# Performance work log

Hardware: AMD Instinct MI355X
Metric: run time of the kernel (lower is better)

Reference implementation:

```python
import jax, jax.numpy as jnp
import numpy as np

N, E = 100000, 1600000
IN_C, HID_C, OUT_C = 128, 64, 40


def setup_inputs() -> dict:
    key = jax.random.key(0)
    ks = jax.random.split(key, 8)
    s = lambda fan_in: 1.0 / np.sqrt(fan_in)
    return {
        "x": jax.random.normal(ks[0], (N, IN_C), dtype=jnp.float32),
        "edge_index": jax.random.randint(ks[1], (2, E), 0, N, dtype=jnp.int64),
        # SAGEConv layer 1: lin_l (on aggregated neighbors, with bias) + lin_r (root, no bias)
        "W_l1": jax.random.uniform(ks[2], (IN_C, HID_C), jnp.float32, -s(IN_C), s(IN_C)),
        "b_l1": jnp.zeros((HID_C,), jnp.float32),
        "W_r1": jax.random.uniform(ks[3], (IN_C, HID_C), jnp.float32, -s(IN_C), s(IN_C)),
        # SAGEConv layer 2
        "W_l2": jax.random.uniform(ks[4], (HID_C, OUT_C), jnp.float32, -s(HID_C), s(HID_C)),
        "b_l2": jnp.zeros((OUT_C,), jnp.float32),
        "W_r2": jax.random.uniform(ks[5], (HID_C, OUT_C), jnp.float32, -s(HID_C), s(HID_C)),
    }


def _sage_conv(x, src, dst, W_l, b_l, W_r, n_nodes):
    # mean-aggregate neighbor features: scatter-add x[src] onto dst, divide by degree
    agg = jax.ops.segment_sum(x[src], dst, num_segments=n_nodes)  # [N, F]
    deg = jax.ops.segment_sum(jnp.ones((src.shape[0],), x.dtype), dst, num_segments=n_nodes)
    mean = agg / jnp.maximum(deg, 1.0)[:, None]
    return mean @ W_l + b_l + x @ W_r


def reference(x, edge_index, W_l1, b_l1, W_r1, W_l2, b_l2, W_r2):
    src, dst = edge_index[0], edge_index[1]  # messages flow src -> dst
    # eval mode: dropout is identity
    hid = _sage_conv(x, src, dst, W_l1, b_l1, W_r1, N)
    hid = jax.nn.relu(hid)
    out = _sage_conv(hid, src, dst, W_l2, b_l2, W_r2, N)
    return jax.nn.log_softmax(out, axis=1)
```

## Files before the change

kernel.cpp:

```cpp
#include <hip/hip_runtime.h>
#include <hip/hip_bf16.h>

#define N_NODES 100000
#define E_EDGES 1600000
#define IN_C 128
#define HID_C 64
#define OUT_C 40

#define NBUCK 196
#define BCAP 9216
#define B1_EPT 16
#define B1_CHUNK (256 * B1_EPT)
#define B1_GRID ((E_EDGES + B1_CHUNK - 1) / B1_CHUNK)
#define TILE_GRID ((N_NODES + 63) / 64)

typedef unsigned short ushort_t;
typedef unsigned int uint_t;
typedef unsigned char uchar_t;
typedef __attribute__((ext_vector_type(8))) short bf16x8;
typedef __attribute__((ext_vector_type(4))) float f32x4;
typedef __attribute__((ext_vector_type(2))) float f32x2;

__device__ __forceinline__ float bfu2f(ushort_t u) {
    return __uint_as_float(((uint_t)u) << 16);
}
__device__ __forceinline__ ushort_t f2bfu(float f) {
    uint_t u = __float_as_uint(f);
    return (ushort_t)((u + 0x7FFFu + ((u >> 16) & 1u)) >> 16);
}
__device__ __forceinline__ uchar_t f2fp8(float f) {
    int p = __builtin_amdgcn_cvt_pk_fp8_f32(f, f, 0, false);
    return (uchar_t)(p & 0xff);
}

struct SmemPrep {
    int cnt[NBUCK];
    int base[NBUCK];
};
struct SmemGemm1 {
    ushort_t xs[64 * 136];
    ushort_t wsm[128 * 136];
};
union SmemK1 {
    SmemPrep p;
    SmemGemm1 g;
};

__global__ __launch_bounds__(256) void k_prep_gemm1(const int* __restrict__ src, const int* __restrict__ dst,
                                                    int* __restrict__ bcur, int* __restrict__ bucket,
                                                    const float* __restrict__ Wl1, const float* __restrict__ Wr1,
                                                    const float* __restrict__ x,
                                                    uchar_t* __restrict__ h1l, ushort_t* __restrict__ h1r) {
    __shared__ SmemK1 sm;
    const int t = threadIdx.x;

    if (blockIdx.x < B1_GRID) {
        const int e0 = blockIdx.x * B1_CHUNK;
        for (int i = t; i < NBUCK; i += 256) sm.p.cnt[i] = 0;
        __syncthreads();

        int myp[B1_EPT];
        int myb[B1_EPT];
#pragma unroll
        for (int j = 0; j < B1_EPT; ++j) {
            int e = e0 + t + j * 256;
            if (e < E_EDGES) {
                int d = dst[e];
                myp[j] = src[e] | ((d & 511) << 17);
                myb[j] = d >> 9;
                atomicAdd(&sm.p.cnt[myb[j]], 1);
            } else {
                myb[j] = -1;
            }
        }
        __syncthreads();
        for (int i = t; i < NBUCK; i += 256) {
            sm.p.base[i] = atomicAdd(&bcur[i], sm.p.cnt[i]);
            sm.p.cnt[i] = 0;
        }
        __syncthreads();
#pragma unroll
        for (int j = 0; j < B1_EPT; ++j) {
            if (myb[j] >= 0) {
                int b = myb[j];
                int loc = atomicAdd(&sm.p.cnt[b], 1);
                int pos = sm.p.base[b] + loc;
                if (pos < BCAP) bucket[(size_t)b * BCAP + pos] = myp[j];
            }
        }
    } else {
        const int row_base = (blockIdx.x - B1_GRID) * 64;

        for (int i = t; i < 128 * 64; i += 256) {
            int n = i & 127, kp = i >> 7;
            const float* W = (n < 64) ? Wl1 : Wr1;
            int nn = n & 63;
            float va = W[(2 * kp) * 64 + nn];
            float vb = W[(2 * kp + 1) * 64 + nn];
            uint_t u = (uint_t)f2bfu(va) | ((uint_t)f2bfu(vb) << 16);
            *(uint_t*)(sm.g.wsm + n * 136 + 2 * kp) = u;
        }
        for (int i = t; i < 64 * 32; i += 256) {
            int row = i >> 5, seg = i & 31;
            int gr = row_base + row;
            float4 v = make_float4(0.f, 0.f, 0.f, 0.f);
            if (gr < N_NODES) v = *(const float4*)(x + (size_t)gr * IN_C + seg * 4);
            ushort4 u;
            u.x = f2bfu(v.x); u.y = f2bfu(v.y); u.z = f2bfu(v.z); u.w = f2bfu(v.w);
            *(ushort4*)(sm.g.xs + row * 136 + seg * 4) = u;
        }
        __syncthreads();

        const int wv = t >> 6, lane = t & 63;
        const int m = lane & 15, quad = lane >> 4;
        const int m0 = wv * 16;

        bf16x8 a[4];
#pragma unroll
        for (int kk = 0; kk < 4; ++kk)
            a[kk] = *(const bf16x8*)(sm.g.xs + (m0 + m) * 136 + kk * 32 + quad * 8);

        f32x4 acc[8];
#pragma unroll
        for (int nt = 0; nt < 8; ++nt) acc[nt] = (f32x4){0.f, 0.f, 0.f, 0.f};

#pragma unroll
        for (int nt = 0; nt < 8; ++nt) {
#pragma unroll
            for (int kk = 0; kk < 4; ++kk) {
                bf16x8 b = *(const bf16x8*)(sm.g.wsm + (nt * 16 + m) * 136 + kk * 32 + quad * 8);
                acc[nt] = __builtin_amdgcn_mfma_f32_16x16x32_bf16(a[kk], b, acc[nt], 0, 0, 0);
            }
        }

        const int grow_base = row_base + m0 + quad * 4;
#pragma unroll
        for (int r = 0; r < 4; ++r) {
            int grow = grow_base + r;
            if (grow < N_NODES) {
#pragma unroll
                for (int nt = 0; nt < 4; ++nt)
                    h1l[(size_t)grow * HID_C + nt * 16 + m] = f2fp8(acc[nt][r]);
#pragma unroll
                for (int nt = 4; nt < 8; ++nt)
                    h1r[(size_t)grow * HID_C + (nt - 4) * 16 + m] = f2bfu(acc[nt][r]);
            }
        }
    }
}

__global__ __launch_bounds__(512) void k_csr(const int* __restrict__ bucket, const int* __restrict__ bcur,
                                             int* __restrict__ rowptr, int* __restrict__ csr,
                                             const float* __restrict__ Wl2, const float* __restrict__ Wr2,
                                             ushort_t* __restrict__ Wt2) {
    const int t = threadIdx.x;
    if (blockIdx.x >= NBUCK) {
        int i = (blockIdx.x - NBUCK) * 512 + t;
        if (i < 80 * 64) {
            int n = i >> 6, k = i & 63;
            float v = (n < 40) ? Wl2[k * 40 + n] : Wr2[k * 40 + (n - 40)];
            Wt2[n * 64 + k] = f2bfu(v);
        }
        return;
    }

    __shared__ int red[512];
    __shared__ int hist[512];
    __shared__ int scan[512];
    __shared__ int cur[512];
    __shared__ int csrbuf[BCAP];

    const int b = blockIdx.x;
    const int n0 = b << 9;
    const int nb = min(512, N_NODES - n0);
    const int sz = min(bcur[b], BCAP);
    const int* bdata = bucket + (size_t)b * BCAP;

    red[t] = (t < b) ? min(bcur[t], BCAP) : 0;
    __syncthreads();
    for (int off = 256; off > 0; off >>= 1) {
        if (t < off) red[t] += red[t + off];
        __syncthreads();
    }
    const int cbase = red[0];

    hist[t] = 0;
    __syncthreads();
    for (int i = t; i < sz; i += 512) atomicAdd(&hist[bdata[i] >> 17], 1);
    __syncthreads();

    scan[t] = hist[t];
    __syncthreads();
    for (int off = 1; off < 512; off <<= 1) {
        int add = (t >= off) ? scan[t - off] : 0;
        __syncthreads();
        scan[t] += add;
        __syncthreads();
    }

    int exc = scan[t] - hist[t];
    cur[t] = exc;
    if (t < nb) rowptr[n0 + t] = cbase + exc;
    __syncthreads();

    for (int i = t; i < sz; i += 512) {
        int p = bdata[i];
        int pos = atomicAdd(&cur[p >> 17], 1);
        csrbuf[pos] = (p & 0x1FFFF) << 6;
    }
    __syncthreads();
    for (int i = t; i < sz; i += 512)
        csr[cbase + i] = csrbuf[i];
    if (b == NBUCK - 1 && t == 0) rowptr[N_NODES] = cbase + sz;
}

__global__ __launch_bounds__(256) void k_agg1_gemm2(const int* __restrict__ rowptr, const int* __restrict__ csr,
                                                    const uchar_t* __restrict__ h1l, const ushort_t* __restrict__ h1r,
                                                    const float* __restrict__ b1, const ushort_t* __restrict__ Wt,
                                                    uchar_t* __restrict__ h2l, ushort_t* __restrict__ h2r) {
    __shared__ ushort_t hs[64 * 72];
    __shared__ ushort_t wsm[80 * 72];
    const int t = threadIdx.x;
    const int row_base = blockIdx.x * 64;
    const int wv = t >> 6, lane = t & 63;
    const int slot = lane >> 3;
    const int part = lane & 7;

    for (int i = t; i < 80 * 8; i += 256) {
        int n = i >> 3, seg = i & 7;
        uint4 v = *(const uint4*)(Wt + n * 64 + seg * 8);
        *(uint4*)(wsm + n * 72 + seg * 8) = v;
    }

    float4 bb0, bb1;
    if (slot == 0) {
        bb0 = *(const float4*)(b1 + part * 8);
        bb1 = *(const float4*)(b1 + part * 8 + 4);
    }
    for (int r16 = 0; r16 < 16; ++r16) {
        int lrow = wv * 16 + r16;
        int row = row_base + lrow;
        if (row < N_NODES) {
            int2 rp = *(const int2*)(rowptr + row);
            int start = rp.x, end = rp.y;
            f32x2 acc[4];
#pragma unroll
            for (int j = 0; j < 4; ++j) acc[j] = (f32x2){0.f, 0.f};

            int base = start;
            for (; base + 8 <= end; base += 8) {
                int s = csr[base + slot];
                uint2 u = *(const uint2*)(h1l + s + part * 8);
                acc[0] += __builtin_amdgcn_cvt_pk_f32_fp8(u.x, false);
                acc[1] += __builtin_amdgcn_cvt_pk_f32_fp8(u.x, true);
                acc[2] += __builtin_amdgcn_cvt_pk_f32_fp8(u.y, false);
                acc[3] += __builtin_amdgcn_cvt_pk_f32_fp8(u.y, true);
            }
            if (base < end) {
                int e = base + slot;
                int s = csr[min(e, end - 1)];
                uint2 u = *(const uint2*)(h1l + s + part * 8);
                if (e >= end) { u.x = 0u; u.y = 0u; }
                acc[0] += __builtin_amdgcn_cvt_pk_f32_fp8(u.x, false);
                acc[1] += __builtin_amdgcn_cvt_pk_f32_fp8(u.x, true);
                acc[2] += __builtin_amdgcn_cvt_pk_f32_fp8(u.y, false);
                acc[3] += __builtin_amdgcn_cvt_pk_f32_fp8(u.y, true);
            }
#pragma unroll
            for (int off = 8; off <= 32; off <<= 1) {
#pragma unroll
                for (int j = 0; j < 4; ++j) {
                    f32x2 tt;
                    tt.x = __shfl_xor(acc[j].x, off);
                    tt.y = __shfl_xor(acc[j].y, off);
                    acc[j] += tt;
                }
            }
            if (slot == 0) {
                float inv = __builtin_amdgcn_rcpf(fmaxf((float)(end - start), 1.0f));
                ushort_t rr[8];
                *(uint4*)rr = *(const uint4*)(h1r + (size_t)row * HID_C + part * 8);
                ushort_t o[8];
                o[0] = f2bfu(fmaxf(acc[0].x * inv + bfu2f(rr[0]) + bb0.x, 0.f));
                o[1] = f2bfu(fmaxf(acc[0].y * inv + bfu2f(rr[1]) + bb0.y, 0.f));
                o[2] = f2bfu(fmaxf(acc[1].x * inv + bfu2f(rr[2]) + bb0.z, 0.f));
                o[3] = f2bfu(fmaxf(acc[1].y * inv + bfu2f(rr[3]) + bb0.w, 0.f));
                o[4] = f2bfu(fmaxf(acc[2].x * inv + bfu2f(rr[4]) + bb1.x, 0.f));
                o[5] = f2bfu(fmaxf(acc[2].y * inv + bfu2f(rr[5]) + bb1.y, 0.f));
                o[6] = f2bfu(fmaxf(acc[3].x * inv + bfu2f(rr[6]) + bb1.z, 0.f));
                o[7] = f2bfu(fmaxf(acc[3].y * inv + bfu2f(rr[7]) + bb1.w, 0.f));
                *(uint4*)(hs + lrow * 72 + part * 8) = *(const uint4*)o;
            }
        } else if (slot == 0) {
            uint4 z = make_uint4(0u, 0u, 0u, 0u);
            *(uint4*)(hs + lrow * 72 + part * 8) = z;
        }
    }
    __syncthreads();

    const int m = lane & 15, quad = lane >> 4;
    const int m0 = wv * 16;

    bf16x8 a[2];
#pragma unroll
    for (int kk = 0; kk < 2; ++kk)
        a[kk] = *(const bf16x8*)(hs + (m0 + m) * 72 + kk * 32 + quad * 8);

    f32x4 acc[5];
#pragma unroll
    for (int nt = 0; nt < 5; ++nt) acc[nt] = (f32x4){0.f, 0.f, 0.f, 0.f};

#pragma unroll
    for (int nt = 0; nt < 5; ++nt) {
#pragma unroll
        for (int kk = 0; kk < 2; ++kk) {
            bf16x8 b = *(const bf16x8*)(wsm + (nt * 16 + m) * 72 + kk * 32 + quad * 8);
            acc[nt] = __builtin_amdgcn_mfma_f32_16x16x32_bf16(a[kk], b, acc[nt], 0, 0, 0);
        }
    }

    const int grow_base = row_base + m0 + quad * 4;
#pragma unroll
    for (int r = 0; r < 4; ++r) {
        int grow = grow_base + r;
        if (grow < N_NODES) {
#pragma unroll
            for (int nt = 0; nt < 5; ++nt) {
                int col = nt * 16 + m;
                float v = acc[nt][r];
                if (col < OUT_C) h2l[(size_t)grow * 64 + col] = f2fp8(v);
                else             h2r[(size_t)grow * OUT_C + (col - OUT_C)] = f2bfu(v);
            }
        }
    }
}

__global__ __launch_bounds__(256) void k_agg2(const int* __restrict__ rowptr, const int* __restrict__ csr,
                                              const uchar_t* __restrict__ h2l, const ushort_t* __restrict__ h2r,
                                              const float* __restrict__ b2, float* __restrict__ out) {
    int row = (blockIdx.x * 256 + threadIdx.x) >> 6;
    int lane = threadIdx.x & 63;
    if (row >= N_NODES) return;
    int2 rp = *(const int2*)(rowptr + row);
    int start = rp.x, end = rp.y;
    const int slot = lane >> 3;
    const int part = lane & 7;
    f32x2 acc[4];
#pragma unroll
    for (int j = 0; j < 4; ++j) acc[j] = (f32x2){0.f, 0.f};

    int base = start;
    for (; base + 8 <= end; base += 8) {
        int s = csr[base + slot];
        uint2 u = *(const uint2*)(h2l + s + part * 8);
        acc[0] += __builtin_amdgcn_cvt_pk_f32_fp8(u.x, false);
        acc[1] += __builtin_amdgcn_cvt_pk_f32_fp8(u.x, true);
        acc[2] += __builtin_amdgcn_cvt_pk_f32_fp8(u.y, false);
        acc[3] += __builtin_amdgcn_cvt_pk_f32_fp8(u.y, true);
    }
    if (base < end) {
        int e = base + slot;
        int s = csr[min(e, end - 1)];
        uint2 u = *(const uint2*)(h2l + s + part * 8);
        if (e >= end) { u.x = 0u; u.y = 0u; }
        acc[0] += __builtin_amdgcn_cvt_pk_f32_fp8(u.x, false);
        acc[1] += __builtin_amdgcn_cvt_pk_f32_fp8(u.x, true);
        acc[2] += __builtin_amdgcn_cvt_pk_f32_fp8(u.y, false);
        acc[3] += __builtin_amdgcn_cvt_pk_f32_fp8(u.y, true);
    }
#pragma unroll
    for (int off = 8; off <= 32; off <<= 1) {
#pragma unroll
        for (int j = 0; j < 4; ++j) {
            f32x2 tt;
            tt.x = __shfl_xor(acc[j].x, off);
            tt.y = __shfl_xor(acc[j].y, off);
            acc[j] += tt;
        }
    }

    const bool fin = (slot == 0) && (part < 5);
    float inv = __builtin_amdgcn_rcpf(fmaxf((float)(end - start), 1.0f));
    f32x2 v2[4];
    if (fin) {
        size_t bi = (size_t)row * OUT_C + part * 8;
        ushort_t rr[8];
        *(uint2*)&rr[0] = *(const uint2*)(h2r + bi);
        *(uint2*)&rr[4] = *(const uint2*)(h2r + bi + 4);
        float4 bb0 = *(const float4*)(b2 + part * 8);
        float4 bb1 = *(const float4*)(b2 + part * 8 + 4);
        v2[0] = (f32x2){acc[0].x * inv + bfu2f(rr[0]) + bb0.x, acc[0].y * inv + bfu2f(rr[1]) + bb0.y};
        v2[1] = (f32x2){acc[1].x * inv + bfu2f(rr[2]) + bb0.z, acc[1].y * inv + bfu2f(rr[3]) + bb0.w};
        v2[2] = (f32x2){acc[2].x * inv + bfu2f(rr[4]) + bb1.x, acc[2].y * inv + bfu2f(rr[5]) + bb1.y};
        v2[3] = (f32x2){acc[3].x * inv + bfu2f(rr[6]) + bb1.z, acc[3].y * inv + bfu2f(rr[7]) + bb1.w};
    } else {
#pragma unroll
        for (int j = 0; j < 4; ++j) v2[j] = (f32x2){-1e30f, -1e30f};
    }
    f32x2 m2;
    m2.x = fmaxf(fmaxf(v2[0].x, v2[1].x), fmaxf(v2[2].x, v2[3].x));
    m2.y = fmaxf(fmaxf(v2[0].y, v2[1].y), fmaxf(v2[2].y, v2[3].y));
    float pm = fmaxf(m2.x, m2.y);
#pragma unroll
    for (int off = 1; off <= 4; off <<= 1) pm = fmaxf(pm, __shfl_xor(pm, off));
    float es = 0.f;
#pragma unroll
    for (int j = 0; j < 4; ++j) {
        es += __expf(v2[j].x - pm);
        es += __expf(v2[j].y - pm);
    }
#pragma unroll
    for (int off = 1; off <= 4; off <<= 1) es += __shfl_xor(es, off);
    float ls = __logf(es);
    if (fin) {
        size_t bo = (size_t)row * OUT_C + part * 8;
        *(float4*)(out + bo) = make_float4(v2[0].x - pm - ls, v2[0].y - pm - ls,
                                           v2[1].x - pm - ls, v2[1].y - pm - ls);
        *(float4*)(out + bo + 4) = make_float4(v2[2].x - pm - ls, v2[2].y - pm - ls,
                                               v2[3].x - pm - ls, v2[3].y - pm - ls);
    }
}

extern "C" void kernel_launch(void* const* d_in, const int* in_sizes, int n_in,
                              void* d_out, int out_size, void* d_ws, size_t ws_size,
                              hipStream_t stream) {
    const float* x   = (const float*)d_in[0];
    const int*   ei  = (const int*)d_in[1];
    const float* Wl1 = (const float*)d_in[2];
    const float* b1  = (const float*)d_in[3];
    const float* Wr1 = (const float*)d_in[4];
    const float* Wl2 = (const float*)d_in[5];
    const float* b2  = (const float*)d_in[6];
    const float* Wr2 = (const float*)d_in[7];

    size_t u = 0;
    int*      bucket = (int*)d_ws;             u += (size_t)NBUCK * BCAP;
    int*      bcur   = (int*)d_ws + u;         u += NBUCK + 4;
    int*      rowptr = (int*)d_ws + u;         u += N_NODES + 1;
    int*      csr    = (int*)d_ws + u;         u += E_EDGES;
    u = (u + 3) & ~(size_t)3;
    ushort_t* Wt2    = (ushort_t*)((int*)d_ws + u); u += 80 * 64 / 2;
    uchar_t*  h1l    = (uchar_t*)((int*)d_ws + u);  u += (size_t)N_NODES * HID_C / 4;
    ushort_t* h1r    = (ushort_t*)((int*)d_ws + u); u += (size_t)N_NODES * HID_C / 2;
    uchar_t*  h2l    = (uchar_t*)((int*)d_ws + u);  u += (size_t)N_NODES * 64 / 4;
    ushort_t* h2r    = (ushort_t*)((int*)d_ws + u); u += (size_t)N_NODES * OUT_C / 2;
    if (ws_size < u * 4) return;

    hipMemsetAsync(bcur, 0, NBUCK * sizeof(int), stream);

    const int* src = ei;
    const int* dst = ei + E_EDGES;

    k_prep_gemm1<<<B1_GRID + TILE_GRID, 256, 0, stream>>>(src, dst, bcur, bucket, Wl1, Wr1, x, h1l, h1r);
    k_csr<<<NBUCK + 10, 512, 0, stream>>>(bucket, bcur, rowptr, csr, Wl2, Wr2, Wt2);
    k_agg1_gemm2<<<TILE_GRID, 256, 0, stream>>>(rowptr, csr, h1l, h1r, b1, Wt2, h2l, h2r);
    k_agg2<<<N_NODES / 4, 256, 0, stream>>>(rowptr, csr, h2l, h2r, b2, (float*)d_out);
}
```

Before: 264.6 us.

## Build CSR via global degree histogram, scan, and atomic scatter instead of buckets

Replaces the bucketed two-pass CSR construction with a per-node degree count via global atomics, a per-512-node block scan, and a direct atomic scatter of edges into CSR positions. It removes the intermediate bucket buffer and its capacity limit. The weight transpose moves into the first kernel. It adds many global atomics and uncoalesced scattered writes, and neighbour order within a row becomes nondeterministic.

```diff
diff --git a/kernel.cpp b/kernel.cpp
--- a/kernel.cpp
+++ b/kernel.cpp
@@ -8,11 +8,11 @@
 #define OUT_C 40
 
 #define NBUCK 196
-#define BCAP 9216
 #define B1_EPT 16
 #define B1_CHUNK (256 * B1_EPT)
 #define B1_GRID ((E_EDGES + B1_CHUNK - 1) / B1_CHUNK)
 #define TILE_GRID ((N_NODES + 63) / 64)
+#define WT2_GRID 20
 
 typedef unsigned short ushort_t;
 typedef unsigned int uint_t;
@@ -33,62 +33,47 @@
     return (uchar_t)(p & 0xff);
 }
 
-struct SmemPrep {
+struct SmemHist {
     int cnt[NBUCK];
-    int base[NBUCK];
 };
 struct SmemGemm1 {
     ushort_t xs[64 * 136];
     ushort_t wsm[128 * 136];
 };
 union SmemK1 {
-    SmemPrep p;
+    SmemHist h;
     SmemGemm1 g;
 };
 
-__global__ __launch_bounds__(256) void k_prep_gemm1(const int* __restrict__ src, const int* __restrict__ dst,
-                                                    int* __restrict__ bcur, int* __restrict__ bucket,
+__global__ __launch_bounds__(256) void k_hist_gemm1(const int* __restrict__ dst,
+                                                    int* __restrict__ deg, int* __restrict__ bcur,
                                                     const float* __restrict__ Wl1, const float* __restrict__ Wr1,
+                                                    const float* __restrict__ Wl2, const float* __restrict__ Wr2,
                                                     const float* __restrict__ x,
-                                                    uchar_t* __restrict__ h1l, ushort_t* __restrict__ h1r) {
+                                                    uchar_t* __restrict__ h1l, ushort_t* __restrict__ h1r,
+                                                    ushort_t* __restrict__ Wt2) {
     __shared__ SmemK1 sm;
     const int t = threadIdx.x;
 
     if (blockIdx.x < B1_GRID) {
         const int e0 = blockIdx.x * B1_CHUNK;
-        for (int i = t; i < NBUCK; i += 256) sm.p.cnt[i] = 0;
-        __syncthreads();
-
-        int myp[B1_EPT];
-        int myb[B1_EPT];
+        for (int i = t; i < NBUCK; i += 256) sm.h.cnt[i] = 0;
+        __syncthreads();
 #pragma unroll
         for (int j = 0; j < B1_EPT; ++j) {
             int e = e0 + t + j * 256;
             if (e < E_EDGES) {
                 int d = dst[e];
-                myp[j] = src[e] | ((d & 511) << 17);
-                myb[j] = d >> 9;
-                atomicAdd(&sm.p.cnt[myb[j]], 1);
-            } else {
-                myb[j] = -1;
+                atomicAdd(&deg[d], 1);
+                atomicAdd(&sm.h.cnt[d >> 9], 1);
             }
         }
         __syncthreads();
         for (int i = t; i < NBUCK; i += 256) {
-            sm.p.base[i] = atomicAdd(&bcur[i], sm.p.cnt[i]);
-            sm.p.cnt[i] = 0;
-        }
-        __syncthreads();
-#pragma unroll
-        for (int j = 0; j < B1_EPT; ++j) {
-            if (myb[j] >= 0) {
-                int b = myb[j];
-                int loc = atomicAdd(&sm.p.cnt[b], 1);
-                int pos = sm.p.base[b] + loc;
-                if (pos < BCAP) bucket[(size_t)b * BCAP + pos] = myp[j];
-            }
-        }
-    } else {
+            int c = sm.h.cnt[i];
+            if (c) atomicAdd(&bcur[i], c);
+        }
+    } else if (blockIdx.x < B1_GRID + TILE_GRID) {
         const int row_base = (blockIdx.x - B1_GRID) * 64;
 
         for (int i = t; i < 128 * 64; i += 256) {
@@ -146,37 +131,25 @@
                     h1r[(size_t)grow * HID_C + (nt - 4) * 16 + m] = f2bfu(acc[nt][r]);
             }
         }
-    }
-}
-
-__global__ __launch_bounds__(512) void k_csr(const int* __restrict__ bucket, const int* __restrict__ bcur,
-                                             int* __restrict__ rowptr, int* __restrict__ csr,
-                                             const float* __restrict__ Wl2, const float* __restrict__ Wr2,
-                                             ushort_t* __restrict__ Wt2) {
-    const int t = threadIdx.x;
-    if (blockIdx.x >= NBUCK) {
-        int i = (blockIdx.x - NBUCK) * 512 + t;
+    } else {
+        int i = (blockIdx.x - B1_GRID - TILE_GRID) * 256 + t;
         if (i < 80 * 64) {
             int n = i >> 6, k = i & 63;
             float v = (n < 40) ? Wl2[k * 40 + n] : Wr2[k * 40 + (n - 40)];
             Wt2[n * 64 + k] = f2bfu(v);
         }
-        return;
-    }
-
+    }
+}
+
+__global__ __launch_bounds__(512) void k_scan(const int* __restrict__ bcur, const int* __restrict__ deg,
+                                              int* __restrict__ B) {
     __shared__ int red[512];
-    __shared__ int hist[512];
-    __shared__ int scan[512];
-    __shared__ int cur[512];
-    __shared__ int csrbuf[BCAP];
-
-    const int b = blockIdx.x;
+    __shared__ int sc[512];
+    const int t = threadIdx.x, b = blockIdx.x;
     const int n0 = b << 9;
     const int nb = min(512, N_NODES - n0);
-    const int sz = min(bcur[b], BCAP);
-    const int* bdata = bucket + (size_t)b * BCAP;
-
-    red[t] = (t < b) ? min(bcur[t], BCAP) : 0;
+
+    red[t] = (t < b) ? bcur[t] : 0;
     __syncthreads();
     for (int off = 256; off > 0; off >>= 1) {
         if (t < off) red[t] += red[t + off];
@@ -184,34 +157,32 @@
     }
     const int cbase = red[0];
 
-    hist[t] = 0;
-    __syncthreads();
-    for (int i = t; i < sz; i += 512) atomicAdd(&hist[bdata[i] >> 17], 1);
-    __syncthreads();
-
-    scan[t] = hist[t];
+    int d = (t < nb) ? deg[n0 + t] : 0;
+    sc[t] = d;
     __syncthreads();
     for (int off = 1; off < 512; off <<= 1) {
-        int add = (t >= off) ? scan[t - off] : 0;
-        __syncthreads();
-        scan[t] += add;
-        __syncthreads();
-    }
-
-    int exc = scan[t] - hist[t];
-    cur[t] = exc;
-    if (t < nb) rowptr[n0 + t] = cbase + exc;
-    __syncthreads();
-
-    for (int i = t; i < sz; i += 512) {
-        int p = bdata[i];
-        int pos = atomicAdd(&cur[p >> 17], 1);
-        csrbuf[pos] = (p & 0x1FFFF) << 6;
-    }
-    __syncthreads();
-    for (int i = t; i < sz; i += 512)
-        csr[cbase + i] = csrbuf[i];
-    if (b == NBUCK - 1 && t == 0) rowptr[N_NODES] = cbase + sz;
+        int add = (t >= off) ? sc[t - off] : 0;
+        __syncthreads();
+        sc[t] += add;
+        __syncthreads();
+    }
+    if (t < nb) B[n0 + t + 1] = cbase + sc[t] - d;
+    if (b == 0 && t == 0) B[0] = 0;
+}
+
+__global__ __launch_bounds__(256) void k_scatter(const int* __restrict__ src, const int* __restrict__ dst,
+                                                 int* __restrict__ B, int* __restrict__ csr) {
+    const int e0 = blockIdx.x * B1_CHUNK;
+#pragma unroll
+    for (int j = 0; j < B1_EPT; ++j) {
+        int e = e0 + threadIdx.x + j * 256;
+        if (e < E_EDGES) {
+            int s = src[e];
+            int d = dst[e];
+            int pos = atomicAdd(&B[d + 1], 1);
+            csr[pos] = s << 6;
+        }
+    }
 }
 
 __global__ __launch_bounds__(256) void k_agg1_gemm2(const int* __restrict__ rowptr, const int* __restrict__ csr,
@@ -434,9 +405,9 @@
     const float* Wr2 = (const float*)d_in[7];
 
     size_t u = 0;
-    int*      bucket = (int*)d_ws;             u += (size_t)NBUCK * BCAP;
+    int*      deg    = (int*)d_ws;             u += N_NODES;
     int*      bcur   = (int*)d_ws + u;         u += NBUCK + 4;
-    int*      rowptr = (int*)d_ws + u;         u += N_NODES + 1;
+    int*      B      = (int*)d_ws + u;         u += N_NODES + 1;
     int*      csr    = (int*)d_ws + u;         u += E_EDGES;
     u = (u + 3) & ~(size_t)3;
     ushort_t* Wt2    = (ushort_t*)((int*)d_ws + u); u += 80 * 64 / 2;
@@ -446,13 +417,15 @@
     ushort_t* h2r    = (ushort_t*)((int*)d_ws + u); u += (size_t)N_NODES * OUT_C / 2;
     if (ws_size < u * 4) return;
 
-    hipMemsetAsync(bcur, 0, NBUCK * sizeof(int), stream);
+    hipMemsetAsync(deg, 0, (N_NODES + NBUCK + 4) * sizeof(int), stream);
 
     const int* src = ei;
     const int* dst = ei + E_EDGES;
 
-    k_prep_gemm1<<<B1_GRID + TILE_GRID, 256, 0, stream>>>(src, dst, bcur, bucket, Wl1, Wr1, x, h1l, h1r);
-    k_csr<<<NBUCK + 10, 512, 0, stream>>>(bucket, bcur, rowptr, csr, Wl2, Wr2, Wt2);
-    k_agg1_gemm2<<<TILE_GRID, 256, 0, stream>>>(rowptr, csr, h1l, h1r, b1, Wt2, h2l, h2r);
-    k_agg2<<<N_NODES / 4, 256, 0, stream>>>(rowptr, csr, h2l, h2r, b2, (float*)d_out);
-}
+    k_hist_gemm1<<<B1_GRID + TILE_GRID + WT2_GRID, 256, 0, stream>>>(dst, deg, bcur,
+                                                                     Wl1, Wr1, Wl2, Wr2, x, h1l, h1r, Wt2);
+    k_scan<<<NBUCK, 512, 0, stream>>>(bcur, deg, B);
+    k_scatter<<<B1_GRID, 256, 0, stream>>>(src, dst, B, csr);
+    k_agg1_gemm2<<<TILE_GRID, 256, 0, stream>>>(B, csr, h1l, h1r, b1, Wt2, h2l, h2r);
+    k_agg2<<<N_NODES / 4, 256, 0, stream>>>(B, csr, h2l, h2r, b2, (float*)d_out);
+}
```

Measured after the change: 410.8 us. +55.3%, slower.

## Fuse CSR build with layer-1 aggregation and second GEMM using 128-node buckets

Applied to the files above, without the earlier changes.

Dst buckets shrink from 512 to 128 nodes, so each block of the merged kernel builds its CSR slice in shared memory and then aggregates layer 1 straight from that buffer. It also runs the second GEMM for the same 128 rows. The Wt2 transpose moves into the first kernel, which removes one launch and the global round-trip of csr and rowptr before aggregation. In exchange there are more buckets with a smaller capacity per bucket, so overflow is more likely, and the larger shared-memory footprint per block may lower occupancy.

```diff
diff --git a/kernel.cpp b/kernel.cpp
--- a/kernel.cpp
+++ b/kernel.cpp
@@ -7,12 +7,13 @@
 #define HID_C 64
 #define OUT_C 40
 
-#define NBUCK 196
-#define BCAP 9216
+#define NB 782
+#define BCAP 2560
 #define B1_EPT 16
 #define B1_CHUNK (256 * B1_EPT)
-#define B1_GRID ((E_EDGES + B1_CHUNK - 1) / B1_CHUNK)
+#define EB_GRID ((E_EDGES + B1_CHUNK - 1) / B1_CHUNK)
 #define TILE_GRID ((N_NODES + 63) / 64)
+#define WT2_GRID 20
 
 typedef unsigned short ushort_t;
 typedef unsigned int uint_t;
@@ -33,9 +34,17 @@
     return (uchar_t)(p & 0xff);
 }
 
+#define ACC8(A, U)                                                   \
+    do {                                                             \
+        (A)[0] += __builtin_amdgcn_cvt_pk_f32_fp8((U).x, false);     \
+        (A)[1] += __builtin_amdgcn_cvt_pk_f32_fp8((U).x, true);      \
+        (A)[2] += __builtin_amdgcn_cvt_pk_f32_fp8((U).y, false);     \
+        (A)[3] += __builtin_amdgcn_cvt_pk_f32_fp8((U).y, true);      \
+    } while (0)
+
 struct SmemPrep {
-    int cnt[NBUCK];
-    int base[NBUCK];
+    int cnt[NB];
+    int base[NB];
 };
 struct SmemGemm1 {
     ushort_t xs[64 * 136];
@@ -49,14 +58,16 @@
 __global__ __launch_bounds__(256) void k_prep_gemm1(const int* __restrict__ src, const int* __restrict__ dst,
                                                     int* __restrict__ bcur, int* __restrict__ bucket,
                                                     const float* __restrict__ Wl1, const float* __restrict__ Wr1,
+                                                    const float* __restrict__ Wl2, const float* __restrict__ Wr2,
                                                     const float* __restrict__ x,
-                                                    uchar_t* __restrict__ h1l, ushort_t* __restrict__ h1r) {
+                                                    uchar_t* __restrict__ h1l, ushort_t* __restrict__ h1r,
+                                                    ushort_t* __restrict__ Wt2) {
     __shared__ SmemK1 sm;
     const int t = threadIdx.x;
 
-    if (blockIdx.x < B1_GRID) {
+    if (blockIdx.x < EB_GRID) {
         const int e0 = blockIdx.x * B1_CHUNK;
-        for (int i = t; i < NBUCK; i += 256) sm.p.cnt[i] = 0;
+        for (int i = t; i < NB; i += 256) sm.p.cnt[i] = 0;
         __syncthreads();
 
         int myp[B1_EPT];
@@ -66,15 +77,15 @@
             int e = e0 + t + j * 256;
             if (e < E_EDGES) {
                 int d = dst[e];
-                myp[j] = src[e] | ((d & 511) << 17);
-                myb[j] = d >> 9;
+                myp[j] = src[e] | ((d & 127) << 17);
+                myb[j] = d >> 7;
                 atomicAdd(&sm.p.cnt[myb[j]], 1);
             } else {
                 myb[j] = -1;
             }
         }
         __syncthreads();
-        for (int i = t; i < NBUCK; i += 256) {
+        for (int i = t; i < NB; i += 256) {
             sm.p.base[i] = atomicAdd(&bcur[i], sm.p.cnt[i]);
             sm.p.cnt[i] = 0;
         }
@@ -88,8 +99,8 @@
                 if (pos < BCAP) bucket[(size_t)b * BCAP + pos] = myp[j];
             }
         }
-    } else {
-        const int row_base = (blockIdx.x - B1_GRID) * 64;
+    } else if (blockIdx.x < EB_GRID + TILE_GRID) {
+        const int row_base = (blockIdx.x - EB_GRID) * 64;
 
         for (int i = t; i < 128 * 64; i += 256) {
             int n = i & 127, kp = i >> 7;
@@ -146,37 +157,46 @@
                     h1r[(size_t)grow * HID_C + (nt - 4) * 16 + m] = f2bfu(acc[nt][r]);
             }
         }
-    }
-}
-
-__global__ __launch_bounds__(512) void k_csr(const int* __restrict__ bucket, const int* __restrict__ bcur,
-                                             int* __restrict__ rowptr, int* __restrict__ csr,
-                                             const float* __restrict__ Wl2, const float* __restrict__ Wr2,
-                                             ushort_t* __restrict__ Wt2) {
-    const int t = threadIdx.x;
-    if (blockIdx.x >= NBUCK) {
-        int i = (blockIdx.x - NBUCK) * 512 + t;
+    } else {
+        int i = (blockIdx.x - EB_GRID - TILE_GRID) * 256 + t;
         if (i < 80 * 64) {
             int n = i >> 6, k = i & 63;
             float v = (n < 40) ? Wl2[k * 40 + n] : Wr2[k * 40 + (n - 40)];
             Wt2[n * 64 + k] = f2bfu(v);
         }
-        return;
-    }
-
+    }
+}
+
+__global__ __launch_bounds__(512) void k_csr_agg1_gemm2(const int* __restrict__ bcur, const int* __restrict__ bucket,
+                                                        const uchar_t* __restrict__ h1l, const ushort_t* __restrict__ h1r,
+                                                        const float* __restrict__ b1, const ushort_t* __restrict__ Wt,
+                                                        int* __restrict__ rowptr, int* __restrict__ csr,
+                                                        uchar_t* __restrict__ h2l, ushort_t* __restrict__ h2r) {
     __shared__ int red[512];
-    __shared__ int hist[512];
-    __shared__ int scan[512];
-    __shared__ int cur[512];
+    __shared__ int hist[128];
+    __shared__ int excl[128];
+    __shared__ int cur[128];
     __shared__ int csrbuf[BCAP];
-
+    __shared__ ushort_t hs[128 * 72];
+    __shared__ ushort_t wsm[80 * 72];
+
+    const int t = threadIdx.x;
     const int b = blockIdx.x;
-    const int n0 = b << 9;
-    const int nb = min(512, N_NODES - n0);
+    const int n0 = b << 7;
+    const int nb = min(128, N_NODES - n0);
     const int sz = min(bcur[b], BCAP);
-    const int* bdata = bucket + (size_t)b * BCAP;
-
-    red[t] = (t < b) ? min(bcur[t], BCAP) : 0;
+    const int* __restrict__ bdata = bucket + (size_t)b * BCAP;
+
+    for (int i = t; i < 80 * 8; i += 512) {
+        int nn = i >> 3, seg = i & 7;
+        *(uint4*)(wsm + nn * 72 + seg * 8) = *(const uint4*)(Wt + nn * 64 + seg * 8);
+    }
+
+    {
+        int v = 0;
+        for (int i = t; i < b; i += 512) v += min(bcur[i], BCAP);
+        red[t] = v;
+    }
     __syncthreads();
     for (int off = 256; off > 0; off >>= 1) {
         if (t < off) red[t] += red[t + off];
@@ -184,23 +204,26 @@
     }
     const int cbase = red[0];
 
-    hist[t] = 0;
+    if (t < 128) hist[t] = 0;
     __syncthreads();
     for (int i = t; i < sz; i += 512) atomicAdd(&hist[bdata[i] >> 17], 1);
     __syncthreads();
 
-    scan[t] = hist[t];
-    __syncthreads();
-    for (int off = 1; off < 512; off <<= 1) {
-        int add = (t >= off) ? scan[t - off] : 0;
-        __syncthreads();
-        scan[t] += add;
-        __syncthreads();
-    }
-
-    int exc = scan[t] - hist[t];
-    cur[t] = exc;
-    if (t < nb) rowptr[n0 + t] = cbase + exc;
+    if (t < 128) red[t] = hist[t];
+    __syncthreads();
+    int pp = 0;
+    for (int off = 1; off < 128; off <<= 1) {
+        if (t < 128) red[(1 - pp) * 128 + t] = red[pp * 128 + t] + ((t >= off) ? red[pp * 128 + t - off] : 0);
+        __syncthreads();
+        pp ^= 1;
+    }
+    if (t < 128) {
+        int ex = red[pp * 128 + t] - hist[t];
+        excl[t] = ex;
+        cur[t] = ex;
+        if (t < nb) rowptr[n0 + t] = cbase + ex;
+    }
+    if (b == NB - 1 && t == 0) rowptr[N_NODES] = cbase + sz;
     __syncthreads();
 
     for (int i = t; i < sz; i += 512) {
@@ -211,27 +234,10 @@
     __syncthreads();
     for (int i = t; i < sz; i += 512)
         csr[cbase + i] = csrbuf[i];
-    if (b == NBUCK - 1 && t == 0) rowptr[N_NODES] = cbase + sz;
-}
-
-__global__ __launch_bounds__(256) void k_agg1_gemm2(const int* __restrict__ rowptr, const int* __restrict__ csr,
-                                                    const uchar_t* __restrict__ h1l, const ushort_t* __restrict__ h1r,
-                                                    const float* __restrict__ b1, const ushort_t* __restrict__ Wt,
-                                                    uchar_t* __restrict__ h2l, ushort_t* __restrict__ h2r) {
-    __shared__ ushort_t hs[64 * 72];
-    __shared__ ushort_t wsm[80 * 72];
-    const int t = threadIdx.x;
-    const int row_base = blockIdx.x * 64;
+
     const int wv = t >> 6, lane = t & 63;
     const int slot = lane >> 3;
     const int part = lane & 7;
-
-    for (int i = t; i < 80 * 8; i += 256) {
-        int n = i >> 3, seg = i & 7;
-        uint4 v = *(const uint4*)(Wt + n * 64 + seg * 8);
-        *(uint4*)(wsm + n * 72 + seg * 8) = v;
-    }
-
     float4 bb0, bb1;
     if (slot == 0) {
         bb0 = *(const float4*)(b1 + part * 8);
@@ -239,32 +245,26 @@
     }
     for (int r16 = 0; r16 < 16; ++r16) {
         int lrow = wv * 16 + r16;
-        int row = row_base + lrow;
+        int row = n0 + lrow;
         if (row < N_NODES) {
-            int2 rp = *(const int2*)(rowptr + row);
-            int start = rp.x, end = rp.y;
+            int start = excl[lrow];
+            int end = start + hist[lrow];
             f32x2 acc[4];
 #pragma unroll
             for (int j = 0; j < 4; ++j) acc[j] = (f32x2){0.f, 0.f};
 
             int base = start;
             for (; base + 8 <= end; base += 8) {
-                int s = csr[base + slot];
+                int s = csrbuf[base + slot];
                 uint2 u = *(const uint2*)(h1l + s + part * 8);
-                acc[0] += __builtin_amdgcn_cvt_pk_f32_fp8(u.x, false);
-                acc[1] += __builtin_amdgcn_cvt_pk_f32_fp8(u.x, true);
-                acc[2] += __builtin_amdgcn_cvt_pk_f32_fp8(u.y, false);
-                acc[3] += __builtin_amdgcn_cvt_pk_f32_fp8(u.y, true);
+                ACC8(acc, u);
             }
             if (base < end) {
                 int e = base + slot;
-                int s = csr[min(e, end - 1)];
+                int s = csrbuf[min(e, end - 1)];
                 uint2 u = *(const uint2*)(h1l + s + part * 8);
                 if (e >= end) { u.x = 0u; u.y = 0u; }
-                acc[0] += __builtin_amdgcn_cvt_pk_f32_fp8(u.x, false);
-                acc[1] += __builtin_amdgcn_cvt_pk_f32_fp8(u.x, true);
-                acc[2] += __builtin_amdgcn_cvt_pk_f32_fp8(u.y, false);
-                acc[3] += __builtin_amdgcn_cvt_pk_f32_fp8(u.y, true);
+                ACC8(acc, u);
             }
 #pragma unroll
             for (int off = 8; off <= 32; off <<= 1) {
@@ -299,27 +299,27 @@
     __syncthreads();
 
     const int m = lane & 15, quad = lane >> 4;
-    const int m0 = wv * 16;
+    const int row0 = wv * 16;
 
     bf16x8 a[2];
 #pragma unroll
     for (int kk = 0; kk < 2; ++kk)
-        a[kk] = *(const bf16x8*)(hs + (m0 + m) * 72 + kk * 32 + quad * 8);
-
-    f32x4 acc[5];
-#pragma unroll
-    for (int nt = 0; nt < 5; ++nt) acc[nt] = (f32x4){0.f, 0.f, 0.f, 0.f};
+        a[kk] = *(const bf16x8*)(hs + (row0 + m) * 72 + kk * 32 + quad * 8);
+
+    f32x4 acg[5];
+#pragma unroll
+    for (int nt = 0; nt < 5; ++nt) acg[nt] = (f32x4){0.f, 0.f, 0.f, 0.f};
 
 #pragma unroll
     for (int nt = 0; nt < 5; ++nt) {
 #pragma unroll
         for (int kk = 0; kk < 2; ++kk) {
-            bf16x8 b = *(const bf16x8*)(wsm + (nt * 16 + m) * 72 + kk * 32 + quad * 8);
-            acc[nt] = __builtin_amdgcn_mfma_f32_16x16x32_bf16(a[kk], b, acc[nt], 0, 0, 0);
-        }
-    }
-
-    const int grow_base = row_base + m0 + quad * 4;
+            bf16x8 bb = *(const bf16x8*)(wsm + (nt * 16 + m) * 72 + kk * 32 + quad * 8);
+            acg[nt] = __builtin_amdgcn_mfma_f32_16x16x32_bf16(a[kk], bb, acg[nt], 0, 0, 0);
+        }
+    }
+
+    const int grow_base = n0 + row0 + quad * 4;
 #pragma unroll
     for (int r = 0; r < 4; ++r) {
         int grow = grow_base + r;
@@ -327,7 +327,7 @@
 #pragma unroll
             for (int nt = 0; nt < 5; ++nt) {
                 int col = nt * 16 + m;
-                float v = acc[nt][r];
+                float v = acg[nt][r];
                 if (col < OUT_C) h2l[(size_t)grow * 64 + col] = f2fp8(v);
                 else             h2r[(size_t)grow * OUT_C + (col - OUT_C)] = f2bfu(v);
             }
@@ -353,20 +353,14 @@
     for (; base + 8 <= end; base += 8) {
         int s = csr[base + slot];
         uint2 u = *(const uint2*)(h2l + s + part * 8);
-        acc[0] += __builtin_amdgcn_cvt_pk_f32_fp8(u.x, false);
-        acc[1] += __builtin_amdgcn_cvt_pk_f32_fp8(u.x, true);
-        acc[2] += __builtin_amdgcn_cvt_pk_f32_fp8(u.y, false);
-        acc[3] += __builtin_amdgcn_cvt_pk_f32_fp8(u.y, true);
+        ACC8(acc, u);
     }
     if (base < end) {
         int e = base + slot;
         int s = csr[min(e, end - 1)];
         uint2 u = *(const uint2*)(h2l + s + part * 8);
         if (e >= end) { u.x = 0u; u.y = 0u; }
-        acc[0] += __builtin_amdgcn_cvt_pk_f32_fp8(u.x, false);
-        acc[1] += __builtin_amdgcn_cvt_pk_f32_fp8(u.x, true);
-        acc[2] += __builtin_amdgcn_cvt_pk_f32_fp8(u.y, false);
-        acc[3] += __builtin_amdgcn_cvt_pk_f32_fp8(u.y, true);
+        ACC8(acc, u);
     }
 #pragma unroll
     for (int off = 8; off <= 32; off <<= 1) {
@@ -434,8 +428,8 @@
     const float* Wr2 = (const float*)d_in[7];
 
     size_t u = 0;
-    int*      bucket = (int*)d_ws;             u += (size_t)NBUCK * BCAP;
-    int*      bcur   = (int*)d_ws + u;         u += NBUCK + 4;
+    int*      bucket = (int*)d_ws;             u += (size_t)NB * BCAP;
+    int*      bcur   = (int*)d_ws + u;         u += NB + 4;
     int*      rowptr = (int*)d_ws + u;         u += N_NODES + 1;
     int*      csr    = (int*)d_ws + u;         u += E_EDGES;
     u = (u + 3) & ~(size_t)3;
@@ -446,13 +440,13 @@
     ushort_t* h2r    = (ushort_t*)((int*)d_ws + u); u += (size_t)N_NODES * OUT_C / 2;
     if (ws_size < u * 4) return;
 
-    hipMemsetAsync(bcur, 0, NBUCK * sizeof(int), stream);
+    hipMemsetAsync(bcur, 0, (NB + 4) * sizeof(int), stream);
 
     const int* src = ei;
     const int* dst = ei + E_EDGES;
 
-    k_prep_gemm1<<<B1_GRID + TILE_GRID, 256, 0, stream>>>(src, dst, bcur, bucket, Wl1, Wr1, x, h1l, h1r);
-    k_csr<<<NBUCK + 10, 512, 0, stream>>>(bucket, bcur, rowptr, csr, Wl2, Wr2, Wt2);
-    k_agg1_gemm2<<<TILE_GRID, 256, 0, stream>>>(rowptr, csr, h1l, h1r, b1, Wt2, h2l, h2r);
+    k_prep_gemm1<<<EB_GRID + TILE_GRID + WT2_GRID, 256, 0, stream>>>(src, dst, bcur, bucket,
+                                                                     Wl1, Wr1, Wl2, Wr2, x, h1l, h1r, Wt2);
+    k_csr_agg1_gemm2<<<NB, 512, 0, stream>>>(bcur, bucket, h1l, h1r, b1, Wt2, rowptr, csr, h2l, h2r);
     k_agg2<<<N_NODES / 4, 256, 0, stream>>>(rowptr, csr, h2l, h2r, b2, (float*)d_out);
 }
```

Measured after the change: 273.9 us. 1.04x slower.
